# Performance work log

Measured on AMD Instinct MI355X. Metric: run time of the kernel, lower is better.

## Reference

```python
import jax, jax.numpy as jnp
import numpy as np

B, S, D = 8, 8192, 64
N_HASHES = 8
BUCKET_SIZE = 64
N_BUCKETS = S // BUCKET_SIZE  # 128
SELF_ATTN_VALUE = -5e4  # torch reformer TOKEN_SELF_ATTN_VALUE


def setup_inputs() -> dict:
    key = jax.random.key(0)
    k1, k2, k3 = jax.random.split(key, 3)
    qk = jax.random.normal(k1, (B, S, D), dtype=jnp.float32)
    v = jax.random.normal(k2, (B, S, D), dtype=jnp.float32)
    # LSH random rotations: (dim, n_hashes, n_buckets // 2), shared across batch/heads
    rotations = jax.random.normal(k3, (D, N_HASHES, N_BUCKETS // 2), dtype=jnp.float32)
    return {"qk": qk, "v": v, "rotations": rotations, "query_len": S}


def _look_one_back(x):
    # concatenate each chunk with the preceding chunk (wrapping) along the kv axis
    x_extra = jnp.concatenate([x[:, -1:], x[:, :-1]], axis=1)
    return jnp.concatenate([x, x_extra], axis=2)


def _lsh_bucketed_dots(qk, v, rotations):
    batch, seqlen, dim = qk.shape
    n_buckets = seqlen // BUCKET_SIZE
    # --- hash vectors: rotate, concat with negation, argmax -> bucket ids ---
    rotated = jnp.einsum('btf,fhi->bhti', qk, rotations)           # (B, H, S, nb/2)
    rotated = jnp.concatenate([rotated, -rotated], axis=-1)        # (B, H, S, nb)
    buckets = jnp.argmax(rotated, axis=-1)                         # (B, H, S) int
    offsets = (jnp.arange(N_HASHES) * n_buckets)[None, :, None]    # disjoint per round
    buckets = (buckets + offsets).reshape(batch, -1)               # (B, H*S)

    # --- stable bucket sort via composite key (all keys unique) ---
    ticker = jnp.arange(N_HASHES * seqlen)[None, :]                # (1, H*S)
    buckets_and_t = seqlen * buckets + (ticker % seqlen)
    sticker = jnp.argsort(buckets_and_t, axis=-1)                  # sort permutation
    undo_sort = jnp.argsort(sticker, axis=-1)                      # inverse permutation
    st = sticker % seqlen                                          # original token ids

    # --- gather tokens into bucket order ---
    sqk = jnp.take_along_axis(qk, st[..., None], axis=1)           # (B, H*S, D)
    sv = jnp.take_along_axis(v, st[..., None], axis=1)

    n_chunks = N_HASHES * n_buckets
    bq_t = st.reshape(batch, n_chunks, BUCKET_SIZE)                # (B, C, bs)
    bqk = sqk.reshape(batch, n_chunks, BUCKET_SIZE, dim)
    bv = sv.reshape(batch, n_chunks, BUCKET_SIZE, dim)

    bq = bqk
    bk = bqk / (jnp.linalg.norm(bqk, axis=-1, keepdims=True) + 1e-6)  # unit-length keys

    bk = _look_one_back(bk)       # (B, C, 2*bs, D)
    bv = _look_one_back(bv)
    bkv_t = _look_one_back(bq_t)  # (B, C, 2*bs)

    dots = jnp.einsum('buie,buje->buij', bq, bk) * (dim ** -0.5)   # (B, C, bs, 2*bs)
    self_mask = bq_t[:, :, :, None] == bkv_t[:, :, None, :]
    dots = jnp.where(self_mask, SELF_ATTN_VALUE, dots)
    return dots, undo_sort, bv


def reference(qk, v, rotations, query_len):
    batch, seqlen, dim = qk.shape
    dots, undo_sort, bv = _lsh_bucketed_dots(qk, v, rotations)
    dots_logsumexp = jax.nn.logsumexp(dots, axis=-1, keepdims=True)
    p = jnp.exp(dots - dots_logsumexp)                             # per-bucket softmax
    bo = jnp.einsum('buij,buje->buie', p, bv)                      # (B, C, bs, D)
    so = bo.reshape(batch, -1, dim)                                # (B, H*S, D)
    slogits = dots_logsumexp.reshape(batch, -1)                    # (B, H*S)
    # undo the bucket sort
    o = jnp.take_along_axis(so, undo_sort[..., None], axis=1)
    logits = jnp.take_along_axis(slogits, undo_sort, axis=1)
    o = o.reshape(batch, N_HASHES, seqlen, dim)[:, :, :query_len]
    logits = logits.reshape(batch, N_HASHES, seqlen, 1)[:, :, :query_len]
    # combine across hash rounds, weighted by per-round logsumexp
    probs = jnp.exp(logits - jax.nn.logsumexp(logits, axis=1, keepdims=True))
    out = jnp.sum(o * probs, axis=1)                               # (B, query_len, D)
    return out
```

## Files before the change

### kernel.cpp

```cpp
#include <hip/hip_runtime.h>
#include <math.h>

#define B_  8
#define S_  8192
#define D_  64
#define H_  8
#define NB_ 128
#define NC_ 1024
#define REP_CAP 65536
#define T2_ 2e-3f

typedef _Float16 f16x8 __attribute__((ext_vector_type(8)));
typedef _Float16 f16x2 __attribute__((ext_vector_type(2)));
typedef float    f32x4 __attribute__((ext_vector_type(4)));
typedef unsigned int uint_;

#define MFMA16(A, Bv, C) __builtin_amdgcn_mfma_f32_16x16x32_f16(A, Bv, C, 0, 0, 0)

__global__ __launch_bounds__(256) void rot_prep_kernel(
    const float* __restrict__ rot, _Float16* __restrict__ rotHi,
    _Float16* __restrict__ rotLo, float* __restrict__ rotT,
    int* __restrict__ cnt)
{
  __shared__ float rs[64 * 64];
  const int tid = threadIdx.x, h = blockIdx.x;
  if (h == 0 && tid == 0) *cnt = 0;
#pragma unroll
  for (int it = 0; it < 16; ++it) {
    const int f = it * 4 + (tid >> 6), i = tid & 63;
    rs[f * 64 + i] = rot[f * 512 + h * 64 + i];
  }
  __syncthreads();
  const int i = tid & 63, grp = tid >> 6;
  _Float16 hi[16], lo[16];
  float tf[16];
#pragma unroll
  for (int ff = 0; ff < 16; ++ff) {
    const float x = rs[(grp * 16 + ff) * 64 + i];
    tf[ff] = x;
    hi[ff] = (_Float16)x;
    lo[ff] = (_Float16)(x - (float)hi[ff]);
  }
  f16x8* dH = (f16x8*)(rotHi + h * 4096 + i * 64 + grp * 16);
  f16x8* dL = (f16x8*)(rotLo + h * 4096 + i * 64 + grp * 16);
  dH[0] = ((f16x8*)hi)[0]; dH[1] = ((f16x8*)hi)[1];
  dL[0] = ((f16x8*)lo)[0]; dL[1] = ((f16x8*)lo)[1];
  float4* dT = (float4*)(rotT + h * 4096 + i * 64 + grp * 16);
#pragma unroll
  for (int k = 0; k < 4; ++k) dT[k] = ((float4*)tf)[k];
}

__global__ __launch_bounds__(256) void hash_kernel(
    const float* __restrict__ qk, const float* __restrict__ v,
    const _Float16* __restrict__ rotHi, const _Float16* __restrict__ rotLo,
    _Float16* __restrict__ q16, _Float16* __restrict__ kn16,
    _Float16* __restrict__ v16,
    int* __restrict__ bucket, int* __restrict__ cnt, int2* __restrict__ list)
{
  __shared__ _Float16 rH[64 * 72];
  __shared__ _Float16 rL[64 * 72];
  const int tid  = threadIdx.x;
  const int b    = blockIdx.x & 7;
  const int tile = blockIdx.x >> 3;
  const int lane = tid & 63, w = tid >> 6;
  const int m16  = lane & 15, qd = lane >> 4;

  {
    const int gt = b * S_ + tile * 64 + (tid >> 2);
    const int qu = tid & 3;
    const size_t off = (size_t)gt * 64 + qu * 16;
    float x[16];
#pragma unroll
    for (int k = 0; k < 4; ++k) ((float4*)x)[k] = ((const float4*)(qk + off))[k];
    float ss = 0.f;
#pragma unroll
    for (int k = 0; k < 16; ++k) ss = fmaf(x[k], x[k], ss);
    ss += __shfl_xor(ss, 1); ss += __shfl_xor(ss, 2);
    const float inv = 0.125f / (sqrtf(ss) + 1e-6f);
    f16x8 qh[2], kn[2];
#pragma unroll
    for (int j = 0; j < 16; ++j) {
      qh[j >> 3][j & 7] = (_Float16)x[j];
      kn[j >> 3][j & 7] = (_Float16)(x[j] * inv);
    }
    ((f16x8*)(q16  + off))[0] = qh[0]; ((f16x8*)(q16  + off))[1] = qh[1];
    ((f16x8*)(kn16 + off))[0] = kn[0]; ((f16x8*)(kn16 + off))[1] = kn[1];
    float y[16];
#pragma unroll
    for (int k = 0; k < 4; ++k) ((float4*)y)[k] = ((const float4*)(v + off))[k];
    f16x8 vv[2];
#pragma unroll
    for (int j = 0; j < 16; ++j) vv[j >> 3][j & 7] = (_Float16)y[j];
    ((f16x8*)(v16 + off))[0] = vv[0]; ((f16x8*)(v16 + off))[1] = vv[1];
  }

  const int t = tile * 64 + w * 16 + m16;
  f16x8 BH0, BH1, BL0, BL1;
  {
    const float* src = qk + ((size_t)b * S_ + t) * 64 + 8 * qd;
    float x[16];
    ((float4*)x)[0] = ((const float4*)src)[0];
    ((float4*)x)[1] = ((const float4*)(src + 4))[0];
    ((float4*)x)[2] = ((const float4*)(src + 32))[0];
    ((float4*)x)[3] = ((const float4*)(src + 36))[0];
#pragma unroll
    for (int j = 0; j < 8; ++j) {
      const _Float16 h0 = (_Float16)x[j];
      BH0[j] = h0; BL0[j] = (_Float16)(x[j] - (float)h0);
      const _Float16 h1 = (_Float16)x[j + 8];
      BH1[j] = h1; BL1[j] = (_Float16)(x[j + 8] - (float)h1);
    }
  }
  const int srow = tid >> 2, scol = (tid & 3) * 16;
  const uint_ qd16 = (uint_)(qd << 4);

#pragma unroll 1
  for (int h = 0; h < 8; ++h) {
    __syncthreads();
    {
      const _Float16* sH = rotHi + h * 4096 + srow * 64 + scol;
      const _Float16* sL = rotLo + h * 4096 + srow * 64 + scol;
      *(f16x8*)(rH + srow * 72 + scol)     = ((const f16x8*)sH)[0];
      *(f16x8*)(rH + srow * 72 + scol + 8) = ((const f16x8*)sH)[1];
      *(f16x8*)(rL + srow * 72 + scol)     = ((const f16x8*)sL)[0];
      *(f16x8*)(rL + srow * 72 + scol + 8) = ((const f16x8*)sL)[1];
    }
    __syncthreads();

    f32x4 acc[4];
#pragma unroll
    for (int mt = 0; mt < 4; ++mt) acc[mt] = (f32x4){0.f, 0.f, 0.f, 0.f};
#pragma unroll
    for (int mt = 0; mt < 4; ++mt) {
      const _Float16* aH = rH + (16 * mt + m16) * 72 + 8 * qd;
      const _Float16* aL = rL + (16 * mt + m16) * 72 + 8 * qd;
      const f16x8 AH0 = *(const f16x8*)aH;
      const f16x8 AH1 = *(const f16x8*)(aH + 32);
      const f16x8 AL0 = *(const f16x8*)aL;
      const f16x8 AL1 = *(const f16x8*)(aL + 32);
      acc[mt] = MFMA16(AH0, BH0, acc[mt]);
      acc[mt] = MFMA16(AH1, BH1, acc[mt]);
      acc[mt] = MFMA16(AH0, BL0, acc[mt]);
      acc[mt] = MFMA16(AH1, BL1, acc[mt]);
      acc[mt] = MFMA16(AL0, BH0, acc[mt]);
      acc[mt] = MFMA16(AL1, BH1, acc[mt]);
    }

    float v1M = -1e30f, v2M = -1e30f, v1m = 1e30f, v2m = 1e30f;
#pragma unroll
    for (int mt = 0; mt < 4; ++mt)
#pragma unroll
      for (int rg = 0; rg < 4; ++rg) {
        uint_ u = __float_as_uint(acc[mt][rg]);
        u = (u & 0xFFFFFFC0u) | qd16 | (uint_)((mt << 2) | rg);
        const float xk = __uint_as_float(u);
        v2M = __builtin_amdgcn_fmed3f(v1M, v2M, xk);
        v1M = fmaxf(v1M, xk);
        v2m = __builtin_amdgcn_fmed3f(v1m, v2m, xk);
        v1m = fminf(v1m, xk);
      }
#pragma unroll
    for (int off = 16; off <= 32; off <<= 1) {
      const float o1M = __shfl_xor(v1M, off), o2M = __shfl_xor(v2M, off);
      v2M = __builtin_amdgcn_fmed3f(v1M, o1M, fmaxf(v2M, o2M));
      v1M = fmaxf(v1M, o1M);
      const float o1m = __shfl_xor(v1m, off), o2m = __shfl_xor(v2m, off);
      v2m = __builtin_amdgcn_fmed3f(v1m, o1m, fminf(v2m, o2m));
      v1m = fminf(v1m, o1m);
    }
    if (qd == 0) {
      const uint_ cM = __float_as_uint(v1M) & 63u;
      const uint_ cm = __float_as_uint(v1m) & 63u;
      const int ixM = 16 * (int)((cM >> 2) & 3u) + 4 * (int)(cM >> 4) + (int)(cM & 3u);
      const int ixm = 16 * (int)((cm >> 2) & 3u) + 4 * (int)(cm >> 4) + (int)(cm & 3u);
      const int bkt = (v1M >= -v1m) ? ixM : 64 + ixm;
      bucket[((size_t)(b * 8 + h)) * S_ + t] = bkt;
      const bool flag = ((v1M - v2M) < T2_) | ((v2m - v1m) < T2_) |
                        (fabsf(v1M + v1m) < T2_);
      if (flag) {
        const int s = atomicAdd(cnt, 1);
        if (s < REP_CAP) list[s] = make_int2(b * 8 + h, t);
      }
    }
  }
}

__global__ __launch_bounds__(256) void repair_kernel(
    const float* __restrict__ qk, const float* __restrict__ rotT,
    const int* __restrict__ cnt, const int2* __restrict__ list,
    int* __restrict__ bucket)
{
  const int n = min(*cnt, REP_CAP);
  const int lane = threadIdx.x & 63;
  const int wid  = (blockIdx.x * 256 + threadIdx.x) >> 6;
  const int nw   = gridDim.x * 4;
  for (int idx = wid; idx < n; idx += nw) {
    const int bh = list[idx].x, t = list[idx].y;
    const int b = bh >> 3, hh = bh & 7;
    const float* qrow = qk + ((size_t)b * S_ + t) * D_;
    const float* rcol = rotT + hh * 4096 + lane * 64;
    double acc = 0.0;
#pragma unroll
    for (int f0 = 0; f0 < 64; f0 += 4) {
      const float4 rq = *(const float4*)(qrow + f0);
      const float4 rc = *(const float4*)(rcol + f0);
      acc = fma((double)rq.x, (double)rc.x, acc);
      acc = fma((double)rq.y, (double)rc.y, acc);
      acc = fma((double)rq.z, (double)rc.z, acc);
      acc = fma((double)rq.w, (double)rc.w, acc);
    }
    double vM = acc; int iM = lane;
    double vm = acc; int im = lane;
#pragma unroll
    for (int off = 32; off >= 1; off >>= 1) {
      const double voM = __shfl_xor(vM, off); const int ioM = __shfl_xor(iM, off);
      if (voM > vM || (voM == vM && ioM < iM)) { vM = voM; iM = ioM; }
      const double vom = __shfl_xor(vm, off); const int iom = __shfl_xor(im, off);
      if (vom < vm || (vom == vm && iom < im)) { vm = vom; im = iom; }
    }
    if (lane == 0) {
      const int bkt = (vM >= -vm) ? iM : 64 + im;
      bucket[(size_t)bh * S_ + t] = bkt;
    }
  }
}

__global__ __launch_bounds__(1024) void sort_kernel(
    const int* __restrict__ bucket, int* __restrict__ st)
{
  __shared__ uint_ hist[64 * 128];
  __shared__ unsigned short lb[S_];
  __shared__ int off[128];
  __shared__ int wtot;
  const int tid = threadIdx.x;
  const int bh  = blockIdx.x;
  const size_t base = (size_t)bh * S_;

#pragma unroll
  for (int k = 0; k < 8; ++k) hist[tid + k * 1024] = 0;
  __syncthreads();

#pragma unroll
  for (int k = 0; k < 8; ++k) {
    const int t = k * 1024 + tid;
    const int bk = bucket[base + t];
    lb[t] = (unsigned short)bk;
    const int g = t >> 6;
    atomicAdd(&hist[(g & 63) * 128 + bk], 1u << (16 * (g >> 6)));
  }
  __syncthreads();

  int s = 0;
  if (tid < 128) {
#pragma unroll
    for (int g = 0; g < 64; ++g) {
      const uint_ wv = hist[g * 128 + tid];
      s += (int)((wv & 0xFFFFu) + (wv >> 16));
    }
  }
  int x = s;
#pragma unroll
  for (int d = 1; d < 64; d <<= 1) {
    const int y = __shfl_up(x, d);
    if ((tid & 63) >= d) x += y;
  }
  if (tid == 63) wtot = x;
  __syncthreads();
  if (tid < 128) {
    if (tid >= 64) x += wtot;
    off[tid] = x - s;
  }
  __syncthreads();

  if (tid < 128) {
    uint_ run = (uint_)off[tid];
#pragma unroll
    for (int g = 0; g < 64; ++g) {
      const uint_ wv = hist[g * 128 + tid];
      hist[g * 128 + tid] = (wv & 0xFFFF0000u) | run;
      run += (wv & 0xFFFFu);
    }
#pragma unroll
    for (int g = 0; g < 64; ++g) {
      const uint_ wv = hist[g * 128 + tid];
      hist[g * 128 + tid] = (wv & 0xFFFFu) | (run << 16);
      run += (wv >> 16);
    }
  }
  __syncthreads();

  const int lane = tid & 63, wv_ = tid >> 6;
  const int b = bh >> 3, h = bh & 7;
  const size_t stb = (size_t)b * (H_ * S_) + (size_t)h * S_;
  const unsigned long long ltmask = (1ull << lane) - 1ull;
#pragma unroll
  for (int k = 0; k < 8; ++k) {
    const int g = wv_ * 8 + k;
    const int t = g * 64 + lane;
    const int bk = (int)lb[t];
    unsigned long long same = ~0ull;
#pragma unroll
    for (int bit = 0; bit < 7; ++bit) {
      const unsigned long long m = __ballot((bk >> bit) & 1);
      same &= ((bk >> bit) & 1) ? m : ~m;
    }
    const int rloc = __popcll(same & ltmask);
    const uint_ wd = hist[(g & 63) * 128 + bk];
    const int gbase = (int)((wd >> (16 * (g >> 6))) & 0xFFFFu);
    st[stb + gbase + rloc] = t;
  }
}

__global__ __launch_bounds__(256, 8) void attn_kernel(
    const _Float16* __restrict__ q16, const _Float16* __restrict__ kn16,
    const _Float16* __restrict__ v16, const int* __restrict__ st,
    _Float16* __restrict__ so, float* __restrict__ slog)
{
  __shared__ _Float16 smem[128 * 72];
  __shared__ __align__(16) int sIds[128];

  const int tid = threadIdx.x;
  const int b   = blockIdx.x & 7;
  const int c   = blockIdx.x >> 3;
  const int cm1 = (c + NC_ - 1) & (NC_ - 1);
  const size_t bst = (size_t)b * (H_ * S_);
  const size_t row0 = bst + (size_t)c * 64;
  const size_t row1 = bst + (size_t)cm1 * 64;

  const int lane = tid & 63;
  const int w    = tid >> 6;
  const int m16  = lane & 15;
  const int qd   = lane >> 4;

  if (tid < 128) sIds[tid] = (tid < 64) ? st[row0 + tid] : st[row1 + tid - 64];

  const int rid = st[row0 + 16 * w + m16];
  f16x8 q0, q1;
  {
    const _Float16* qp = q16 + ((size_t)b * S_ + rid) * 64 + 8 * qd;
    q0 = *(const f16x8*)qp;
    q1 = *(const f16x8*)(qp + 32);
  }

  const int r = tid >> 2, qu = tid & 3;
  {
    const int tokA = st[row0 + r];
    const int tokB = st[row1 + r];
    const f16x8* ska = (const f16x8*)(kn16 + ((size_t)b * S_ + tokA) * 64 + qu * 16);
    const f16x8* skb = (const f16x8*)(kn16 + ((size_t)b * S_ + tokB) * 64 + qu * 16);
    *(f16x8*)(smem + r * 72 + qu * 16)            = ska[0];
    *(f16x8*)(smem + r * 72 + qu * 16 + 8)        = ska[1];
    *(f16x8*)(smem + (64 + r) * 72 + qu * 16)     = skb[0];
    *(f16x8*)(smem + (64 + r) * 72 + qu * 16 + 8) = skb[1];
  }
  __syncthreads();

  f32x4 acc[8];
#pragma unroll
  for (int jt = 0; jt < 8; ++jt) acc[jt] = (f32x4){0.f, 0.f, 0.f, 0.f};

  __builtin_amdgcn_s_setprio(1);
#pragma unroll
  for (int jt = 0; jt < 8; ++jt) {
    const _Float16* krow = smem + (16 * jt + m16) * 72;
    const f16x8 kb0 = *(const f16x8*)(krow + 8 * qd);
    const f16x8 kb1 = *(const f16x8*)(krow + 32 + 8 * qd);
    acc[jt] = MFMA16(kb0, q0, acc[jt]);
    acc[jt] = MFMA16(kb1, q1, acc[jt]);
  }
  __builtin_amdgcn_s_setprio(0);

  float m = -1e30f;
#pragma unroll
  for (int jt = 0; jt < 8; ++jt) {
    const int4 cid = *(const int4*)(sIds + 16 * jt + 4 * qd);
    float x;
    x = acc[jt][0]; if (cid.x == rid) x = -5e4f; acc[jt][0] = x; m = fmaxf(m, x);
    x = acc[jt][1]; if (cid.y == rid) x = -5e4f; acc[jt][1] = x; m = fmaxf(m, x);
    x = acc[jt][2]; if (cid.z == rid) x = -5e4f; acc[jt][2] = x; m = fmaxf(m, x);
    x = acc[jt][3]; if (cid.w == rid) x = -5e4f; acc[jt][3] = x; m = fmaxf(m, x);
  }
  m = fmaxf(m, __shfl_xor(m, 16));
  m = fmaxf(m, __shfl_xor(m, 32));
  float sum = 0.f;
#pragma unroll
  for (int jt = 0; jt < 8; ++jt)
#pragma unroll
    for (int rg = 0; rg < 4; ++rg) {
      const float e = __expf(acc[jt][rg] - m);
      acc[jt][rg] = e;
      sum += e;
    }
  sum += __shfl_xor(sum, 16);
  sum += __shfl_xor(sum, 32);
  const float rinv = 1.f / sum;

  const int hh = c >> 7;
  const size_t hb = ((size_t)(b * 8 + hh)) * S_;
  if (qd == 0) slog[hb + rid] = m + __logf(sum);

  f16x8 pa[4];
#pragma unroll
  for (int s = 0; s < 4; ++s)
#pragma unroll
    for (int j = 0; j < 8; ++j)
      pa[s][j] = (_Float16)acc[2 * s + (j >> 2)][j & 3];

  const int c0 = 2 * r;
  const int k0 = 32 * (c0 >> 5) + 16 * ((c0 >> 2) & 1) + 4 * ((c0 >> 3) & 3) + (c0 & 3);
  const int tok0 = sIds[k0], tok1 = sIds[k0 + 1];
  f16x8 va[2], vb[2];
  {
    const f16x8* s0 = (const f16x8*)(v16 + ((size_t)b * S_ + tok0) * 64 + qu * 16);
    const f16x8* s1 = (const f16x8*)(v16 + ((size_t)b * S_ + tok1) * 64 + qu * 16);
    va[0] = s0[0]; va[1] = s0[1];
    vb[0] = s1[0]; vb[1] = s1[1];
  }
  __syncthreads();

  {
    const int swz = (qu << 3) ^ ((qu & 1) << 5);
    _Float16* dst = smem + (c0 ^ swz);
#pragma unroll
    for (int jj = 0; jj < 16; ++jj) {
      const int d = 16 * qu + jj;
      f16x2 pk; pk[0] = va[jj >> 3][jj & 7]; pk[1] = vb[jj >> 3][jj & 7];
      *(f16x2*)(dst + d * 136) = pk;
    }
  }
  __syncthreads();

  f32x4 oacc[4];
#pragma unroll
  for (int dt = 0; dt < 4; ++dt) oacc[dt] = (f32x4){0.f, 0.f, 0.f, 0.f};
  __builtin_amdgcn_s_setprio(1);
#pragma unroll
  for (int s = 0; s < 4; ++s) {
#pragma unroll
    for (int dt = 0; dt < 4; ++dt) {
      const _Float16* vp = smem + (16 * dt + m16) * 136
                         + 32 * (s ^ (dt & 1)) + 8 * (qd ^ dt);
      const f16x8 bv = *(const f16x8*)(vp);
      oacc[dt] = MFMA16(pa[s], bv, oacc[dt]);
    }
  }
  __builtin_amdgcn_s_setprio(0);

  float rin[4];
#pragma unroll
  for (int rg = 0; rg < 4; ++rg) rin[rg] = __shfl(rinv, 4 * qd + rg);

  __syncthreads();
#pragma unroll
  for (int dt = 0; dt < 4; ++dt)
#pragma unroll
    for (int rg = 0; rg < 4; ++rg)
      smem[(16 * w + 4 * qd + rg) * 72 + 16 * dt + m16] =
          (_Float16)(oacc[dt][rg] * rin[rg]);
  __syncthreads();

  {
    const int tok = sIds[r];
    const f16x8* srcp = (const f16x8*)(smem + r * 72 + qu * 16);
    const f16x8 o0 = srcp[0], o1 = srcp[1];
    f16x8* dstp = (f16x8*)(so + (hb + tok) * 64 + qu * 16);
    dstp[0] = o0; dstp[1] = o1;
  }
}

__global__ __launch_bounds__(256) void combine_kernel(
    const _Float16* __restrict__ so, const float* __restrict__ slog,
    float* __restrict__ out)
{
  const int gid = blockIdx.x * 256 + threadIdx.x;
  const int gt  = gid >> 3;
  const int oct = gid & 7;
  const int b   = gt >> 13;
  const int t   = gt & (S_ - 1);
  const size_t base8 = (size_t)(b * 8) * S_ + t;

  float l[8];
#pragma unroll
  for (int h = 0; h < 8; ++h) l[h] = slog[base8 + (size_t)h * S_];
  float m = l[0];
#pragma unroll
  for (int h = 1; h < 8; ++h) m = fmaxf(m, l[h]);
  float wv[8], W = 0.f;
#pragma unroll
  for (int h = 0; h < 8; ++h) { wv[h] = expf(l[h] - m); W += wv[h]; }
  const float iW = 1.f / W;

  float acc[8] = {0.f, 0.f, 0.f, 0.f, 0.f, 0.f, 0.f, 0.f};
#pragma unroll
  for (int h = 0; h < 8; ++h) {
    const f16x8 vv = *(const f16x8*)(so + (base8 + (size_t)h * S_) * 64 + oct * 8);
#pragma unroll
    for (int j = 0; j < 8; ++j) acc[j] = fmaf(wv[h], (float)vv[j], acc[j]);
  }
  float4 o0, o1;
  o0.x = acc[0] * iW; o0.y = acc[1] * iW; o0.z = acc[2] * iW; o0.w = acc[3] * iW;
  o1.x = acc[4] * iW; o1.y = acc[5] * iW; o1.z = acc[6] * iW; o1.w = acc[7] * iW;
  float4* dst = (float4*)(out + (size_t)gt * 64 + oct * 8);
  dst[0] = o0; dst[1] = o1;
}

extern "C" void kernel_launch(void* const* d_in, const int* in_sizes, int n_in,
                              void* d_out, int out_size, void* d_ws, size_t ws_size,
                              hipStream_t stream)
{
  const float* qk  = (const float*)d_in[0];
  const float* v   = (const float*)d_in[1];
  const float* rot = (const float*)d_in[2];
  float* out = (float*)d_out;

  char* ws = (char*)d_ws;
  const size_t MB = 1ull << 20, KB = 1024;
  int*      bucket = (int*)      (ws + 0 * MB);
  int*      st     = (int*)      (ws + 2 * MB);
  float*    slog   = (float*)    (ws + 4 * MB);
  _Float16* q16    = (_Float16*) (ws + 8 * MB);
  _Float16* kn16   = (_Float16*) (ws + 16 * MB);
  _Float16* v16    = (_Float16*) (ws + 24 * MB);
  _Float16* rotHi  = (_Float16*) (ws + 32 * MB);
  _Float16* rotLo  = (_Float16*) (ws + 32 * MB + 64 * KB);
  int*      cnt    = (int*)      (ws + 32 * MB + 128 * KB);
  int2*     list   = (int2*)     (ws + 32 * MB + 192 * KB);
  float*    rotT   = (float*)    (ws + 32 * MB + 768 * KB);
  _Float16* so     = (_Float16*) (ws + 33 * MB);
  if (ws_size < 98 * MB) return;

  hipLaunchKernelGGL(rot_prep_kernel, dim3(8),         dim3(256),  0, stream,
                     rot, rotHi, rotLo, rotT, cnt);
  hipLaunchKernelGGL(hash_kernel,     dim3(8 * 128),   dim3(256),  0, stream,
                     qk, v, rotHi, rotLo, q16, kn16, v16, bucket, cnt, list);
  hipLaunchKernelGGL(repair_kernel,   dim3(128),       dim3(256),  0, stream,
                     qk, rotT, cnt, list, bucket);
  hipLaunchKernelGGL(sort_kernel,     dim3(64),        dim3(1024), 0, stream,
                     bucket, st);
  hipLaunchKernelGGL(attn_kernel,     dim3(B_ * NC_),  dim3(256),  0, stream,
                     q16, kn16, v16, st, so, slog);
  hipLaunchKernelGGL(combine_kernel,  dim3(B_ * S_ * 8 / 256), dim3(256), 0, stream,
                     so, slog, out);
}
```

Before: 180.5 us.

## Prefetch rotation tiles, restructure sort histogram, double repair grid

```diff
diff --git a/kernel.cpp b/kernel.cpp
--- a/kernel.cpp
+++ b/kernel.cpp
@@ -114,17 +114,28 @@
   const int srow = tid >> 2, scol = (tid & 3) * 16;
   const uint_ qd16 = (uint_)(qd << 4);
 
+  f16x8 cH0, cH1, cL0, cL1;
+  {
+    const _Float16* gH = rotHi + srow * 64 + scol;
+    const _Float16* gL = rotLo + srow * 64 + scol;
+    cH0 = ((const f16x8*)gH)[0]; cH1 = ((const f16x8*)gH)[1];
+    cL0 = ((const f16x8*)gL)[0]; cL1 = ((const f16x8*)gL)[1];
+  }
+
 #pragma unroll 1
   for (int h = 0; h < 8; ++h) {
     __syncthreads();
-    {
-      const _Float16* sH = rotHi + h * 4096 + srow * 64 + scol;
-      const _Float16* sL = rotLo + h * 4096 + srow * 64 + scol;
-      *(f16x8*)(rH + srow * 72 + scol)     = ((const f16x8*)sH)[0];
-      *(f16x8*)(rH + srow * 72 + scol + 8) = ((const f16x8*)sH)[1];
-      *(f16x8*)(rL + srow * 72 + scol)     = ((const f16x8*)sL)[0];
-      *(f16x8*)(rL + srow * 72 + scol + 8) = ((const f16x8*)sL)[1];
-    }
+    f16x8 nH0, nH1, nL0, nL1;
+    if (h < 7) {
+      const _Float16* gH = rotHi + (h + 1) * 4096 + srow * 64 + scol;
+      const _Float16* gL = rotLo + (h + 1) * 4096 + srow * 64 + scol;
+      nH0 = ((const f16x8*)gH)[0]; nH1 = ((const f16x8*)gH)[1];
+      nL0 = ((const f16x8*)gL)[0]; nL1 = ((const f16x8*)gL)[1];
+    }
+    *(f16x8*)(rH + srow * 72 + scol)     = cH0;
+    *(f16x8*)(rH + srow * 72 + scol + 8) = cH1;
+    *(f16x8*)(rL + srow * 72 + scol)     = cL0;
+    *(f16x8*)(rL + srow * 72 + scol + 8) = cL1;
     __syncthreads();
 
     f32x4 acc[4];
@@ -182,6 +193,7 @@
         if (s < REP_CAP) list[s] = make_int2(b * 8 + h, t);
       }
     }
+    cH0 = nH0; cH1 = nH1; cL0 = nL0; cL1 = nL1;
   }
 }
 
@@ -228,33 +240,48 @@
 __global__ __launch_bounds__(1024) void sort_kernel(
     const int* __restrict__ bucket, int* __restrict__ st)
 {
-  __shared__ uint_ hist[64 * 128];
+  __shared__ uint_ hist32[128 * 67];
   __shared__ unsigned short lb[S_];
   __shared__ int off[128];
   __shared__ int wtot;
+  unsigned short* hist16 = (unsigned short*)hist32;
   const int tid = threadIdx.x;
   const int bh  = blockIdx.x;
   const size_t base = (size_t)bh * S_;
-
-#pragma unroll
-  for (int k = 0; k < 8; ++k) hist[tid + k * 1024] = 0;
-  __syncthreads();
-
+  const int lane = tid & 63;
+  const unsigned long long ltmask = (1ull << lane) - 1ull;
+
+#pragma unroll
+  for (int k = 0; k < 9; ++k) {
+    const int i = k * 1024 + tid;
+    if (i < 128 * 67) hist32[i] = 0;
+  }
+  __syncthreads();
+
+  int rl[8];
 #pragma unroll
   for (int k = 0; k < 8; ++k) {
     const int t = k * 1024 + tid;
     const int bk = bucket[base + t];
     lb[t] = (unsigned short)bk;
-    const int g = t >> 6;
-    atomicAdd(&hist[(g & 63) * 128 + bk], 1u << (16 * (g >> 6)));
+    unsigned long long same = ~0ull;
+#pragma unroll
+    for (int bit = 0; bit < 7; ++bit) {
+      const unsigned long long m = __ballot((bk >> bit) & 1);
+      same &= ((bk >> bit) & 1) ? m : ~m;
+    }
+    rl[k] = __popcll(same & ltmask);
+    if ((same & ltmask) == 0ull)
+      hist16[bk * 134 + (t >> 6)] = (unsigned short)__popcll(same);
   }
   __syncthreads();
 
   int s = 0;
   if (tid < 128) {
-#pragma unroll
-    for (int g = 0; g < 64; ++g) {
-      const uint_ wv = hist[g * 128 + tid];
+    const uint_* row = hist32 + tid * 67;
+#pragma unroll
+    for (int g2 = 0; g2 < 64; ++g2) {
+      const uint_ wv = row[g2];
       s += (int)((wv & 0xFFFFu) + (wv >> 16));
     }
   }
@@ -262,7 +289,7 @@
 #pragma unroll
   for (int d = 1; d < 64; d <<= 1) {
     const int y = __shfl_up(x, d);
-    if ((tid & 63) >= d) x += y;
+    if (lane >= d) x += y;
   }
   if (tid == 63) wtot = x;
   __syncthreads();
@@ -273,41 +300,25 @@
   __syncthreads();
 
   if (tid < 128) {
-    uint_ run = (uint_)off[tid];
-#pragma unroll
-    for (int g = 0; g < 64; ++g) {
-      const uint_ wv = hist[g * 128 + tid];
-      hist[g * 128 + tid] = (wv & 0xFFFF0000u) | run;
-      run += (wv & 0xFFFFu);
-    }
-#pragma unroll
-    for (int g = 0; g < 64; ++g) {
-      const uint_ wv = hist[g * 128 + tid];
-      hist[g * 128 + tid] = (wv & 0xFFFFu) | (run << 16);
-      run += (wv >> 16);
-    }
-  }
-  __syncthreads();
-
-  const int lane = tid & 63, wv_ = tid >> 6;
+    int run = off[tid];
+    unsigned short* rowp = hist16 + tid * 134;
+#pragma unroll
+    for (int g = 0; g < 128; ++g) {
+      const int cg = rowp[g];
+      rowp[g] = (unsigned short)run;
+      run += cg;
+    }
+  }
+  __syncthreads();
+
   const int b = bh >> 3, h = bh & 7;
   const size_t stb = (size_t)b * (H_ * S_) + (size_t)h * S_;
-  const unsigned long long ltmask = (1ull << lane) - 1ull;
 #pragma unroll
   for (int k = 0; k < 8; ++k) {
-    const int g = wv_ * 8 + k;
-    const int t = g * 64 + lane;
+    const int t = k * 1024 + tid;
     const int bk = (int)lb[t];
-    unsigned long long same = ~0ull;
-#pragma unroll
-    for (int bit = 0; bit < 7; ++bit) {
-      const unsigned long long m = __ballot((bk >> bit) & 1);
-      same &= ((bk >> bit) & 1) ? m : ~m;
-    }
-    const int rloc = __popcll(same & ltmask);
-    const uint_ wd = hist[(g & 63) * 128 + bk];
-    const int gbase = (int)((wd >> (16 * (g >> 6))) & 0xFFFFu);
-    st[stb + gbase + rloc] = t;
+    const int gb = (int)hist16[bk * 134 + (t >> 6)];
+    st[stb + gb + rl[k]] = t;
   }
 }
 
@@ -533,7 +544,7 @@
                      rot, rotHi, rotLo, rotT, cnt);
   hipLaunchKernelGGL(hash_kernel,     dim3(8 * 128),   dim3(256),  0, stream,
                      qk, v, rotHi, rotLo, q16, kn16, v16, bucket, cnt, list);
-  hipLaunchKernelGGL(repair_kernel,   dim3(128),       dim3(256),  0, stream,
+  hipLaunchKernelGGL(repair_kernel,   dim3(256),       dim3(256),  0, stream,
                      qk, rotT, cnt, list, bucket);
   hipLaunchKernelGGL(sort_kernel,     dim3(64),        dim3(1024), 0, stream,
                      bucket, st);
```

After: 178.2 us. Within noise of the previous version (-1.3%).
